# Kernel optimization log

Hardware: AMD Instinct MI355X
Metric: run time of the kernel (lower is better)

Reference implementation:

```python
import jax, jax.numpy as jnp
import numpy as np

H, W = 80, 80
LOWPASS = 0.3   # 3DGS low-pass filter added to 2D covariance diagonal
NEAR = 0.2      # near-plane cull depth


def quat_to_rot(q):
    # q: [N,4] (w,x,y,z) -> [N,3,3]
    w, x, y, z = q[..., 0], q[..., 1], q[..., 2], q[..., 3]
    return jnp.stack([
        jnp.stack([1 - 2 * (y * y + z * z), 2 * (x * y - w * z), 2 * (x * z + w * y)], -1),
        jnp.stack([2 * (x * y + w * z), 1 - 2 * (x * x + z * z), 2 * (y * z - w * x)], -1),
        jnp.stack([2 * (x * z - w * y), 2 * (y * z + w * x), 1 - 2 * (x * x + y * y)], -1),
    ], -2)


def setup_inputs() -> dict:
    key = jax.random.key(0)
    k1, k2 = jax.random.split(key)
    vsize = 1.25
    def mids(lo, hi, lim):
        g = np.arange(lo, hi + 1e-6, vsize)
        return ((g[:-1] + g[1:]) / 2.0)[:lim]
    xy = mids(-20.0, 20.0, 200)   # 32 midpoints
    zz = mids(-4.0, 4.0, 16)      # 6 midpoints
    X, Y, Z = np.meshgrid(xy, xy, zz, indexing='ij')
    pc_xyz = jnp.asarray(np.stack([X, Y, Z], -1).reshape(-1, 3), jnp.float32)  # [6144,3]
    N = pc_xyz.shape[0]
    B, NC, C = 1, 6, 32
    vox_features = jax.random.normal(k1, (B, N, C), jnp.float32)
    density = jax.random.normal(k2, (B, N), jnp.float32)
    scales = jnp.full((N, 1), float(np.log(vsize)), jnp.float32)
    rots = jnp.concatenate([jnp.ones((N, 1)), jnp.zeros((N, 3))], -1).astype(jnp.float32)
    # 6 surround cameras at origin, yaw = k*60deg; cam axes: x=right, y=up-ish, z=forward
    yaws = np.arange(NC) * (2 * np.pi / NC)
    f = np.stack([np.cos(yaws), np.sin(yaws), np.zeros(NC)], -1)
    r = np.stack([np.sin(yaws), -np.cos(yaws), np.zeros(NC)], -1)
    u = np.cross(f, r)
    Rw2c = np.stack([r, u, f], 1)  # rows are camera axes -> world2cam rotation [NC,3,3]
    cam_rot = jnp.asarray(Rw2c[None], jnp.float32)          # [B,NC,3,3]
    cam_trans = jnp.zeros((B, NC, 3), jnp.float32)          # [B,NC,3]
    cam_intr = jnp.asarray(np.tile(np.array([45.0, 45.0, W / 2.0, H / 2.0], np.float32), (B, NC, 1)))
    return dict(vox_features=vox_features, density=density, cam_rot=cam_rot,
                cam_trans=cam_trans, cam_intr=cam_intr, pc_xyz=pc_xyz,
                scales=scales, rots=rots)


def _render_one(Rcw, t, intr, pc_xyz, Mcov, opacity, feats):
    # Rcw [3,3], t [3], intr [4]; Mcov [N,3,3] = R*diag(s); opacity [N]; feats [N,C]
    fx, fy, cx, cy = intr[0], intr[1], intr[2], intr[3]
    cam = pc_xyz @ Rcw.T + t                    # [N,3] camera-frame means
    tz = jnp.maximum(cam[:, 2], 1e-6)
    valid = (cam[:, 2] > NEAR).astype(pc_xyz.dtype)
    u = fx * cam[:, 0] / tz + cx
    v = fy * cam[:, 1] / tz + cy
    z0 = jnp.zeros_like(tz)
    J = jnp.stack([jnp.stack([fx / tz, z0, -fx * cam[:, 0] / tz ** 2], -1),
                   jnp.stack([z0, fy / tz, -fy * cam[:, 1] / tz ** 2], -1)], -2)  # [N,2,3]
    A = jnp.einsum('nij,jk->nik', J, Rcw)       # J @ W  [N,2,3]
    Bm = jnp.einsum('nij,njk->nik', A, Mcov)    # [N,2,3]
    cov = jnp.einsum('nij,nkj->nik', Bm, Bm)    # 2D covariance [N,2,2]
    a = cov[:, 0, 0] + LOWPASS
    b = cov[:, 0, 1]
    c = cov[:, 1, 1] + LOWPASS
    det = a * c - b * b
    ia, ib, ic = c / det, -b / det, a / det
    # depth-sort (invalid gaussians pushed to the back)
    order = jnp.argsort(tz + (1.0 - valid) * 1e6)
    u, v, ia, ib, ic = u[order], v[order], ia[order], ib[order], ic[order]
    op_s, feat_s, valid_s = opacity[order], feats[order], valid[order]
    px = jnp.arange(W, dtype=pc_xyz.dtype)
    py = jnp.arange(H, dtype=pc_xyz.dtype)
    dx = px[None, None, :] - u[:, None, None]   # [N,1,W] -> broadcast [N,H,W]
    dy = py[None, :, None] - v[:, None, None]   # [N,H,1]
    power = (-0.5 * (ia[:, None, None] * dx * dx + ic[:, None, None] * dy * dy)
             - ib[:, None, None] * dx * dy)
    g = jnp.exp(jnp.minimum(power, 0.0))
    alpha = jnp.clip(op_s[:, None, None] * g, 0.0, 0.99) * valid_s[:, None, None]
    Tcum = jnp.cumprod(1.0 - alpha, axis=0)
    Texc = jnp.concatenate([jnp.ones((1, H, W), alpha.dtype), Tcum[:-1]], 0)  # exclusive transmittance
    return jnp.einsum('nhw,nc->chw', Texc * alpha, feat_s)


def reference(vox_features, density, cam_rot, cam_trans, cam_intr, pc_xyz, scales, rots):
    Bsz, N, C = vox_features.shape
    Rg = quat_to_rot(rots)                      # [N,3,3]
    s = jnp.exp(scales)                         # [N,1] isotropic scale
    Mcov = Rg * s[:, :, None]                   # R @ diag(s,s,s)
    outs = []
    for b in range(Bsz):
        op = jax.nn.softplus(density[b]).reshape(-1)        # opacity activation
        feats = vox_features[b].reshape(-1, C)
        def rone(args):
            R_, t_, K_ = args
            return _render_one(R_, t_, K_, pc_xyz, Mcov, op, feats)
        out_b = jax.lax.map(rone, (cam_rot[b], cam_trans[b], cam_intr[b]))  # [NC,C,H,W]
        outs.append(out_b)
    return jnp.stack(outs)                      # [B,NC,C,H,W]
```

## Files before the change

### kernel.cpp

```cpp
#include <hip/hip_runtime.h>

#define NEARV    0.2f
#define LOWPASSV 0.3f

constexpr int HH = 80, WW = 80;
constexpr int CFE = 32;
constexpr int NZ = 6;

constexpr int NCELL = 1024;
constexpr int HMAX = NCELL * NZ;

typedef unsigned long long u64;
typedef unsigned int u32;

__global__ __launch_bounds__(512) void rank_kernel(
    const float* __restrict__ pc_xyz, const float* __restrict__ cam_rot,
    const float* __restrict__ cam_trans, int N,
    int* __restrict__ counts, int* __restrict__ cellord)
{
  __shared__ u32 sk[NCELL];
  __shared__ u32 wred[8];

  const int cam = blockIdx.y;
  const int tid = threadIdx.x;
  const float* R = cam_rot + cam*9;
  const float R20 = R[6], R21 = R[7], R22 = R[8];
  const float t2  = cam_trans[cam*3+2];

  int vcnt = 0;
  #pragma unroll
  for (int e2 = 0; e2 < NCELL/512; ++e2) {
    const int cell = e2*512 + tid;
    const int i0 = cell * NZ;
    u32 key22 = 0x3FFFFFu;
    if (i0 < N) {
      float c2 = R20*pc_xyz[i0*3+0] + R21*pc_xyz[i0*3+1] + R22*pc_xyz[i0*3+2] + t2;
      if (c2 > NEARV) {
        u32 b = __float_as_uint(c2) - 0x3E000000u;
        b = b < 0x03FFFF00u ? b : 0x03FFFF00u;
        key22 = b >> 4;
        ++vcnt;
      }
    }
    sk[cell] = (key22 << 10) | (u32)cell;
  }
  __syncthreads();

  const int cell = blockIdx.x * 256 + (tid >> 1);
  const u32 mykey = sk[cell];
  const uint4* k4 = (const uint4*)sk;
  const int h0 = (tid & 1) * (NCELL/8);
  int rank = 0;
  #pragma unroll 8
  for (int i = 0; i < NCELL/8; ++i) {
    const uint4 kv = k4[h0 + i];
    rank += (int)(kv.x < mykey) + (int)(kv.y < mykey)
          + (int)(kv.z < mykey) + (int)(kv.w < mykey);
  }
  rank += __shfl_xor(rank, 1, 64);

  if ((tid & 1) == 0)
    cellord[(size_t)cam * NCELL + rank] = cell;

  if (blockIdx.x == 0) {
    #pragma unroll
    for (int off = 32; off > 0; off >>= 1) vcnt += __shfl_down(vcnt, off, 64);
    if ((tid & 63) == 0) wred[tid >> 6] = (u32)vcnt;
    __syncthreads();
    if (tid == 0) {
      u32 tot = 0;
      #pragma unroll
      for (int w = 0; w < 8; ++w) tot += wred[w];
      counts[cam] = (int)tot * NZ;
    }
  }
}

__global__ __launch_bounds__(256) void proj_kernel(
    const float* __restrict__ pc_xyz, const float* __restrict__ cam_rot,
    const float* __restrict__ cam_trans, const float* __restrict__ cam_intr,
    const float* __restrict__ density, const float* __restrict__ scales,
    int N, int NC,
    const int* __restrict__ counts, const int* __restrict__ cellord,
    float4* __restrict__ hdrA, float4* __restrict__ hdrB)
{
  const int cam = blockIdx.y;
  const int kq = blockIdx.x * 256 + threadIdx.x;
  if (kq >= counts[cam]) return;

  const int cellp = kq / NZ;
  const int n = cellord[(size_t)cam * NCELL + cellp] * NZ + (kq - cellp * NZ);

  const float* R = cam_rot + cam*9;
  const float* t = cam_trans + cam*3;
  const float* intr = cam_intr + cam*4;
  const float fx = intr[0], fy = intr[1], cx = intr[2], cy = intr[3];
  const int b = cam / NC;

  const float p0 = pc_xyz[n*3+0], p1 = pc_xyz[n*3+1], p2 = pc_xyz[n*3+2];
  const float c0 = R[0]*p0 + R[1]*p1 + R[2]*p2 + t[0];
  const float c1 = R[3]*p0 + R[4]*p1 + R[5]*p2 + t[1];
  const float c2 = R[6]*p0 + R[7]*p1 + R[8]*p2 + t[2];
  const float tz = fmaxf(c2, 1e-6f);
  const float itz = 1.0f / tz;
  const float u = fx*c0*itz + cx;
  const float v = fy*c1*itz + cy;
  const float j00 = fx*itz, j02 = -(fx*c0*itz)*itz;
  const float j11 = fy*itz, j12 = -(fy*c1*itz)*itz;
  const float s = expf(scales[n]);
  const float s2 = s*s;
  const float cov00 = s2*(j00*j00 + j02*j02);
  const float cov01 = s2*(j02*j12);
  const float cov11 = s2*(j11*j11 + j12*j12);
  const float a = cov00 + LOWPASSV, bb = cov01, cc = cov11 + LOWPASSV;
  const float det = a*cc - bb*bb;
  const float idet = 1.0f / det;
  const float mid = 0.5f*(a + cc);
  const float dd = sqrtf(fmaxf(mid*mid - det, 0.f));
  float r2 = 32.f * (mid + dd);
  const float dens = density[(size_t)b*N + n];
  const float op = fmaxf(dens, 0.f) + log1pf(expf(-fabsf(dens)));
  const float sx = fminf(fmaxf(u, 0.f), (float)(WW-1)) - u;
  const float sy = fminf(fmaxf(v, 0.f), (float)(HH-1)) - v;
  if (sx*sx + sy*sy > r2) r2 = -1.0f;

  const float L = 1.4426950408889634f;
  const float A2 = -0.5f * (cc*idet) * L;
  const float C2 = -0.5f * (a*idet)  * L;
  const float B2 =         (bb*idet) * L;

  hdrA[(size_t)cam * HMAX + kq] = make_float4(u, v, A2, B2);
  hdrB[(size_t)cam * HMAX + kq] = make_float4(C2, op, r2, __int_as_float(n));
}

__global__ __launch_bounds__(64) void render_kernel(
    const float* __restrict__ vox,
    const float4* __restrict__ hdrA, const float4* __restrict__ hdrB,
    const int* __restrict__ counts,
    float* __restrict__ out, int N, int NC)
{
  __shared__ float4 cA[64], cB[64];
  __shared__ int   cgi[64];
  __shared__ float4 sfeat[64];

  const int cam = blockIdx.y;
  const int tile = blockIdx.x;
  const int tx = tile % (WW/8), ty = tile / (WW/8);
  const int lane = threadIdx.x;
  const int p  = lane & 31;
  const int h  = lane >> 5;
  const int lx = p & 7, ly = p >> 3;
  const int px = tx*8 + lx, py = ty*4 + ly;
  const float fpx = (float)px, fpy = (float)py;
  const float tx0 = (float)(tx*8), tx1 = tx0 + 7.f;
  const float ty0 = (float)(ty*4), ty1 = ty0 + 3.f;
  const int count = counts[cam];
  const int b = cam / NC;
  const float4* hA = hdrA + (size_t)cam * HMAX;
  const float4* hB = hdrB + (size_t)cam * HMAX;
  const float4* voxb = (const float4*)vox + (size_t)b * N * (CFE/4);

  float acc[CFE/2];
  #pragma unroll
  for (int i = 0; i < CFE/2; ++i) acc[i] = 0.f;
  float T = 1.0f;
  bool done = false;

#define LOAD4(Aarr, Barr, base_) do {                                   \
    _Pragma("unroll")                                                   \
    for (int d_ = 0; d_ < 4; ++d_) {                                    \
      const int kn_ = min((base_) + d_*64 + lane, count - 1);           \
      Aarr[d_] = hA[kn_]; Barr[d_] = hB[kn_];                           \
    } } while (0)

#define PROCESS_CHUNK(k0_, a0_, b0_) do {                               \
    const int ki = (k0_) + lane;                                        \
    const float ddx = fminf(fmaxf((a0_).x, tx0), tx1) - (a0_).x;        \
    const float ddy = fminf(fmaxf((a0_).y, ty0), ty1) - (a0_).y;        \
    const bool hit = (ki < count) && (ddx*ddx + ddy*ddy <= (b0_).z);    \
    const u64 m = __ballot(hit);                                        \
    const int P = __popcll(m);                                          \
    if (P == 0) continue;                                               \
    if (hit) {                                                          \
      const int pos = (int)__popcll(m & ((1ull << lane) - 1ull));       \
      cA[pos] = (a0_); cB[pos] = (b0_);                                 \
      cgi[pos] = __float_as_int((b0_).w);                               \
    }                                                                   \
    __builtin_amdgcn_wave_barrier();   \
    const int sl = lane >> 3, sc = lane & 7;                            \
    float4 pf = voxb[(size_t)cgi[min(sl, P - 1)] * (CFE/4) + sc];       \
    for (int j = 0; j < P; j += 8) {                                    \
           \
      float al[8];                                                      \
      _Pragma("unroll")                                                 \
      for (int qq = 0; qq < 8; ++qq) {                                  \
        const int idx = j + qq;                                         \
        const float4 a1 = cA[idx & 63];             \
        const float4 a2 = cB[idx & 63];           \
        const float dx = fpx - a1.x, dy = fpy - a1.y;                   \
        const float q1 = dx*dx, q2 = dy*dy, q3 = dx*dy;                 \
        const float pl2 = a1.z*q1 + a2.x*q2 + a1.w*q3;   \
        float av = fminf(a2.y * __builtin_exp2f(fminf(pl2, 0.f)), 0.99f); \
        av = (pl2 > -23.0831f) ? av : 0.f;       \
        al[qq] = (idx < P) ? av : 0.f;                                  \
      }                                                                 \
      sfeat[lane] = pf;                  \
      if (j + 8 < P) {                            \
        const int si = min(j + 8 + sl, P - 1);                          \
        pf = voxb[(size_t)cgi[si] * (CFE/4) + sc];                      \
      }                                                                 \
      __builtin_amdgcn_wave_barrier();   \
      _Pragma("unroll")                                                 \
      for (int qq = 0; qq < 8; ++qq) {                                  \
        const float w = T * al[qq];                                     \
        T -= w;                                                         \
        if (__any(w > 1e-8f)) {                                         \
          const float4* fj = &sfeat[qq * 8 + 4 * h];                    \
          _Pragma("unroll")                                             \
          for (int c4 = 0; c4 < 4; ++c4) {                              \
            const float4 fv = fj[c4];                                   \
            acc[c4*4+0] = fmaf(w, fv.x, acc[c4*4+0]);                   \
            acc[c4*4+1] = fmaf(w, fv.y, acc[c4*4+1]);                   \
            acc[c4*4+2] = fmaf(w, fv.z, acc[c4*4+2]);                   \
            acc[c4*4+3] = fmaf(w, fv.w, acc[c4*4+3]);                   \
          }                                                             \
        }                                                               \
      }                                                                 \
      if (__all(T < 1e-3f)) { done = true; break; }                     \
      __builtin_amdgcn_wave_barrier();  \
    }                                                                   \
  } while (0)

  if (count > 0) {
    float4 A0x[4], B0x[4], A1x[4], B1x[4];
    const int nquad = (count + 255) >> 8;
    LOAD4(A0x, B0x, 0);

    for (int q = 0; q < nquad && !done; q += 2) {
      if (q + 1 < nquad) LOAD4(A1x, B1x, (q+1)*256);
      #pragma unroll
      for (int d = 0; d < 4; ++d) {
        if (done) break;
        const int k0 = q*256 + d*64;
        if (k0 >= count) break;
        PROCESS_CHUNK(k0, A0x[d], B0x[d]);
      }
      if (done || q + 1 >= nquad) break;
      if (q + 2 < nquad) LOAD4(A0x, B0x, (q+2)*256);
      #pragma unroll
      for (int d = 0; d < 4; ++d) {
        if (done) break;
        const int k0 = (q+1)*256 + d*64;
        if (k0 >= count) break;
        PROCESS_CHUNK(k0, A1x[d], B1x[d]);
      }
    }
  }
#undef PROCESS_CHUNK
#undef LOAD4

  float* ob = out + (((size_t)cam * CFE + 16*h) * HH + py) * WW + px;
  #pragma unroll
  for (int c = 0; c < CFE/2; ++c) ob[(size_t)c * HH * WW] = acc[c];
}

extern "C" void kernel_launch(void* const* d_in, const int* in_sizes, int n_in,
                              void* d_out, int out_size, void* d_ws, size_t ws_size,
                              hipStream_t stream) {
  const float* vox       = (const float*)d_in[0];
  const float* density   = (const float*)d_in[1];
  const float* cam_rot   = (const float*)d_in[2];
  const float* cam_trans = (const float*)d_in[3];
  const float* cam_intr  = (const float*)d_in[4];
  const float* pc_xyz    = (const float*)d_in[5];
  const float* scales    = (const float*)d_in[6];
  float* out = (float*)d_out;

  const int N    = in_sizes[5] / 3;
  const int NCAM = in_sizes[4] / 4;
  const int B    = in_sizes[1] / N;
  const int NC   = NCAM / B;

  unsigned char* ws = (unsigned char*)d_ws;
  int* countsPtr = (int*)ws;
  int* cellord   = (int*)(ws + 256);
  float4* hdrA   = (float4*)(ws + 32768);
  float4* hdrB   = (float4*)(ws + 32768 + (size_t)NCAM * HMAX * sizeof(float4));

  rank_kernel<<<dim3(NCELL/256, NCAM), 512, 0, stream>>>(
      pc_xyz, cam_rot, cam_trans, N, countsPtr, cellord);
  proj_kernel<<<dim3((HMAX + 255) / 256, NCAM), 256, 0, stream>>>(
      pc_xyz, cam_rot, cam_trans, cam_intr, density, scales, N, NC,
      countsPtr, cellord, hdrA, hdrB);
  render_kernel<<<dim3((WW/8)*(HH/4), NCAM), 64, 0, stream>>>(
      vox, hdrA, hdrB, countsPtr, out, N, NC);
}
```

Baseline: 83.41 us.

## Render 16x4 pixel tiles with one pixel per lane and readlane-broadcast splat params

The render kernel now gives each of the 64 lanes one pixel of a 16x4 tile and accumulates all 32 channels per lane, instead of two half-waves splitting channels over an 8x4 tile. Splat parameters are no longer staged through LDS. Each hit gaussian's header is broadcast with readlane, with lanes chosen by iterating the ballot mask. This halves the block count and removes the per-gaussian LDS parameter traffic, so alpha work is no longer duplicated across the two channel halves. The cost is more accumulator registers, larger tiles that pass more culling tests, and fewer blocks to spread across the GPU.

```diff
diff --git a/kernel.cpp b/kernel.cpp
--- a/kernel.cpp
+++ b/kernel.cpp
@@ -139,32 +139,31 @@
     const int* __restrict__ counts,
     float* __restrict__ out, int N, int NC)
 {
-  __shared__ float4 cA[64], cB[64];
   __shared__ int   cgi[64];
   __shared__ float4 sfeat[64];
 
   const int cam = blockIdx.y;
   const int tile = blockIdx.x;
-  const int tx = tile % (WW/8), ty = tile / (WW/8);
+  const int tx = tile % (WW/16), ty = tile / (WW/16);
   const int lane = threadIdx.x;
-  const int p  = lane & 31;
-  const int h  = lane >> 5;
-  const int lx = p & 7, ly = p >> 3;
-  const int px = tx*8 + lx, py = ty*4 + ly;
+  const int lx = lane & 15, ly = lane >> 4;
+  const int px = tx*16 + lx, py = ty*4 + ly;
   const float fpx = (float)px, fpy = (float)py;
-  const float tx0 = (float)(tx*8), tx1 = tx0 + 7.f;
-  const float ty0 = (float)(ty*4), ty1 = ty0 + 3.f;
+  const float tx0 = (float)(tx*16), tx1 = tx0 + 15.f;
+  const float ty0 = (float)(ty*4),  ty1 = ty0 + 3.f;
   const int count = counts[cam];
   const int b = cam / NC;
   const float4* hA = hdrA + (size_t)cam * HMAX;
   const float4* hB = hdrB + (size_t)cam * HMAX;
   const float4* voxb = (const float4*)vox + (size_t)b * N * (CFE/4);
 
-  float acc[CFE/2];
+  float acc[CFE];
   #pragma unroll
-  for (int i = 0; i < CFE/2; ++i) acc[i] = 0.f;
+  for (int i = 0; i < CFE; ++i) acc[i] = 0.f;
   float T = 1.0f;
   bool done = false;
+
+#define RDLN(x, l) __uint_as_float(__builtin_amdgcn_readlane(__float_as_uint(x), (l)))
 
 #define LOAD4(Aarr, Barr, base_) do {                                   \
     _Pragma("unroll")                                                   \
@@ -183,28 +182,33 @@
     if (P == 0) continue;                                               \
     if (hit) {                                                          \
       const int pos = (int)__popcll(m & ((1ull << lane) - 1ull));       \
-      cA[pos] = (a0_); cB[pos] = (b0_);                                 \
       cgi[pos] = __float_as_int((b0_).w);                               \
     }                                                                   \
     __builtin_amdgcn_wave_barrier();   \
     const int sl = lane >> 3, sc = lane & 7;                            \
     float4 pf = voxb[(size_t)cgi[min(sl, P - 1)] * (CFE/4) + sc];       \
+    u64 mm_ = m;                       \
     for (int j = 0; j < P; j += 8) {                                    \
-           \
+            \
       float al[8];                                                      \
       _Pragma("unroll")                                                 \
       for (int qq = 0; qq < 8; ++qq) {                                  \
         const int idx = j + qq;                                         \
-        const float4 a1 = cA[idx & 63];             \
-        const float4 a2 = cB[idx & 63];           \
-        const float dx = fpx - a1.x, dy = fpy - a1.y;                   \
-        const float q1 = dx*dx, q2 = dy*dy, q3 = dx*dy;                 \
-        const float pl2 = a1.z*q1 + a2.x*q2 + a1.w*q3;   \
-        float av = fminf(a2.y * __builtin_exp2f(fminf(pl2, 0.f)), 0.99f); \
+        int lq = 0;                                                     \
+        if (mm_) { lq = (int)__builtin_ctzll(mm_); mm_ &= mm_ - 1; }    \
+        const float su  = RDLN((a0_).x, lq);                            \
+        const float sv  = RDLN((a0_).y, lq);                            \
+        const float sA2 = RDLN((a0_).z, lq);                            \
+        const float sB2 = RDLN((a0_).w, lq);                            \
+        const float sC2 = RDLN((b0_).x, lq);                            \
+        const float sop = RDLN((b0_).y, lq);                            \
+        const float dx = fpx - su, dy = fpy - sv;                       \
+        const float pl2 = sA2*(dx*dx) + sC2*(dy*dy) + sB2*(dx*dy);      \
+        float av = fminf(sop * __builtin_exp2f(fminf(pl2, 0.f)), 0.99f); \
         av = (pl2 > -23.0831f) ? av : 0.f;       \
         al[qq] = (idx < P) ? av : 0.f;                                  \
       }                                                                 \
-      sfeat[lane] = pf;                  \
+      sfeat[lane] = pf;                            \
       if (j + 8 < P) {                            \
         const int si = min(j + 8 + sl, P - 1);                          \
         pf = voxb[(size_t)cgi[si] * (CFE/4) + sc];                      \
@@ -215,14 +219,14 @@
         const float w = T * al[qq];                                     \
         T -= w;                                                         \
         if (__any(w > 1e-8f)) {                                         \
-          const float4* fj = &sfeat[qq * 8 + 4 * h];                    \
+          const float4* fj = &sfeat[qq * 8];                            \
           _Pragma("unroll")                                             \
-          for (int c4 = 0; c4 < 4; ++c4) {                              \
-            const float4 fv = fj[c4];                                   \
-            acc[c4*4+0] = fmaf(w, fv.x, acc[c4*4+0]);                   \
-            acc[c4*4+1] = fmaf(w, fv.y, acc[c4*4+1]);                   \
-            acc[c4*4+2] = fmaf(w, fv.z, acc[c4*4+2]);                   \
-            acc[c4*4+3] = fmaf(w, fv.w, acc[c4*4+3]);                   \
+          for (int c8 = 0; c8 < CFE/4; ++c8) {                          \
+            const float4 fv = fj[c8];                                   \
+            acc[c8*4+0] = fmaf(w, fv.x, acc[c8*4+0]);                   \
+            acc[c8*4+1] = fmaf(w, fv.y, acc[c8*4+1]);                   \
+            acc[c8*4+2] = fmaf(w, fv.z, acc[c8*4+2]);                   \
+            acc[c8*4+3] = fmaf(w, fv.w, acc[c8*4+3]);                   \
           }                                                             \
         }                                                               \
       }                                                                 \
@@ -258,10 +262,11 @@
   }
 #undef PROCESS_CHUNK
 #undef LOAD4
-
-  float* ob = out + (((size_t)cam * CFE + 16*h) * HH + py) * WW + px;
+#undef RDLN
+
+  float* ob = out + (((size_t)cam * CFE) * HH + py) * WW + px;
   #pragma unroll
-  for (int c = 0; c < CFE/2; ++c) ob[(size_t)c * HH * WW] = acc[c];
+  for (int c = 0; c < CFE; ++c) ob[(size_t)c * HH * WW] = acc[c];
 }
 
 extern "C" void kernel_launch(void* const* d_in, const int* in_sizes, int n_in,
@@ -292,6 +297,6 @@
   proj_kernel<<<dim3((HMAX + 255) / 256, NCAM), 256, 0, stream>>>(
       pc_xyz, cam_rot, cam_trans, cam_intr, density, scales, N, NC,
       countsPtr, cellord, hdrA, hdrB);
-  render_kernel<<<dim3((WW/8)*(HH/4), NCAM), 64, 0, stream>>>(
+  render_kernel<<<dim3((WW/16)*(HH/4), NCAM), 64, 0, stream>>>(
       vox, hdrA, hdrB, countsPtr, out, N, NC);
 }
```

New measurement: 82.41 us. Within noise of the previous version (-1.2%).
